# Optimization experiments

Measured on AMD Instinct MI355X. Metric: run time of the kernel, lower is better.

Reference implementation:

```python
import jax, jax.numpy as jnp
import numpy as np

THRESHOLD = 0.5
NEG_POS = 3
ALPHA = 1.0


def cxcy_to_xy(c):
    return jnp.concatenate([c[..., :2] - c[..., 2:] / 2, c[..., :2] + c[..., 2:] / 2], axis=-1)


def xy_to_cxcy(x):
    return jnp.concatenate([(x[..., :2] + x[..., 2:]) / 2, x[..., 2:] - x[..., :2]], axis=-1)


def encode_gcxgcy(cxcy, priors_cxcy):
    # SSD offset encoding with variances (10, 10, 5, 5)
    return jnp.concatenate([
        (cxcy[..., :2] - priors_cxcy[..., :2]) / (priors_cxcy[..., 2:] / 10.0),
        jnp.log(cxcy[..., 2:] / priors_cxcy[..., 2:]) * 5.0,
    ], axis=-1)


def compute_iou(a, b):
    # a: [n,4] xyxy, b: [m,4] xyxy -> [n,m]
    lt = jnp.maximum(a[:, None, :2], b[None, :, :2])
    rb = jnp.minimum(a[:, None, 2:], b[None, :, 2:])
    wh = jnp.clip(rb - lt, 0.0)
    inter = wh[..., 0] * wh[..., 1]
    area_a = (a[:, 2] - a[:, 0]) * (a[:, 3] - a[:, 1])
    area_b = (b[:, 2] - b[:, 0]) * (b[:, 3] - b[:, 1])
    return inter / (area_a[:, None] + area_b[None, :] - inter)


def _match_one(boxes, labels, db_xy, db_cxcy):
    # boxes: [n_obj,4] xyxy, labels: [n_obj], priors: [P,4]
    n_obj = boxes.shape[0]
    overlaps = compute_iou(boxes, db_xy)                 # [n_obj, P]
    ov_per_box = jnp.max(overlaps, axis=0)               # [P]
    obj_per_box = jnp.argmax(overlaps, axis=0)           # [P]
    box_per_obj = jnp.argmax(overlaps, axis=1)           # [n_obj]
    # force each gt to own its best prior
    obj_per_box = obj_per_box.at[box_per_obj].set(jnp.arange(n_obj))
    ov_per_box = ov_per_box.at[box_per_obj].set(1.0)
    lbl = labels[obj_per_box]                            # [P]
    lbl = jnp.where(ov_per_box < THRESHOLD, 0, lbl)      # background below threshold
    true_locs = encode_gcxgcy(xy_to_cxcy(boxes[obj_per_box]), db_cxcy)  # [P,4]
    return true_locs, lbl


def smooth_l1(x):
    ax = jnp.abs(x)
    return jnp.where(ax < 1.0, 0.5 * x * x, ax - 0.5)


def reference(loc_pred, cls_pred, gt_boxes, gt_labels, default_boxes):
    # loc_pred: [B,P,4], cls_pred: [B,P,C], gt_boxes: [B,n_obj,4],
    # gt_labels: [B,n_obj] int, default_boxes: [P,4] cxcywh
    db_xy = cxcy_to_xy(default_boxes)
    true_locs, true_labels = jax.vmap(_match_one, in_axes=(0, 0, None, None))(
        gt_boxes, gt_labels, db_xy, default_boxes)      # [B,P,4], [B,P]

    positive = true_labels > 0                           # [B,P]
    n_pos = jnp.sum(positive, axis=1)                    # [B]
    n_pos_total = jnp.sum(n_pos).astype(loc_pred.dtype)

    # localization loss: SmoothL1 mean over positive box elements
    loc_elem = smooth_l1(loc_pred - true_locs)           # [B,P,4]
    loc_loss = jnp.sum(loc_elem * positive[..., None]) / (n_pos_total * 4.0)

    # confidence loss: cross entropy with 3:1 hard negative mining
    logp = jax.nn.log_softmax(cls_pred, axis=-1)         # [B,P,C]
    ce = -jnp.take_along_axis(logp, true_labels[..., None], axis=-1)[..., 0]  # [B,P]
    conf_pos = jnp.sum(ce * positive)
    ce_neg = jnp.where(positive, 0.0, ce)
    # rank negatives by loss (descending) per image; take top neg_pos * n_pos
    ranks = jnp.argsort(jnp.argsort(-ce_neg, axis=1), axis=1)  # [B,P]
    hard_neg = ranks < (NEG_POS * n_pos)[:, None]
    conf_hard = jnp.sum(ce_neg * hard_neg)
    conf_loss = (conf_pos + conf_hard) / n_pos_total

    return conf_loss + ALPHA * loc_loss


def setup_inputs() -> dict:
    key = jax.random.key(0)
    ks = jax.random.split(key, 8)
    B, P, C, n_obj = 64, 8732, 81, 32

    # priors in cxcywh, valid in [0,1]
    db_cxy = jax.random.uniform(ks[0], (P, 2), minval=0.05, maxval=0.95)
    db_wh = jax.random.uniform(ks[1], (P, 2), minval=0.05, maxval=0.3)
    default_boxes = jnp.concatenate([db_cxy, db_wh], axis=-1).astype(jnp.float32)

    # gt boxes: valid xyxy built from centers and sizes
    g_cxy = jax.random.uniform(ks[2], (B, n_obj, 2), minval=0.2, maxval=0.8)
    g_wh = jax.random.uniform(ks[3], (B, n_obj, 2), minval=0.1, maxval=0.4)
    gt_boxes = jnp.concatenate([g_cxy - g_wh / 2, g_cxy + g_wh / 2], axis=-1).astype(jnp.float32)
    gt_labels = jax.random.randint(ks[4], (B, n_obj), 1, C)

    loc_pred = jax.random.normal(ks[5], (B, P, 4), dtype=jnp.float32) * 0.1
    cls_pred = jax.random.normal(ks[6], (B, P, C), dtype=jnp.float32)

    return {"loc_pred": loc_pred, "cls_pred": cls_pred, "gt_boxes": gt_boxes,
            "gt_labels": gt_labels, "default_boxes": default_boxes}
```

## Files before the change

### kernel.cpp

```cpp
#include <hip/hip_runtime.h>
#include <hip/hip_bf16.h>
#include <math.h>

#define BB 64
#define PP 8732
#define CC 81
#define NOBJ 32
#define CHUNKS ((PP + 255) / 256)
#define NPRI (BB * PP)
#define WTILE 16
#define WTW (WTILE * CC)
#define NWT (NPRI / WTILE)
#define CE_BLOCKS 1792

typedef float f4 __attribute__((ext_vector_type(4)));

__device__ __forceinline__ float sl1(float x) {
    float ax = fabsf(x);
    return (ax < 1.0f) ? 0.5f * x * x : ax - 0.5f;
}

__global__ __launch_bounds__(256) void k_bestprior(
    const float* __restrict__ gt_boxes,
    const float* __restrict__ dbox,
    int*   __restrict__ bp,
    float* __restrict__ acc,
    int*   __restrict__ npt,
    int*   __restrict__ done,
    int*   __restrict__ n_pos)
{
    __shared__ float s_bv[4];
    __shared__ int   s_bi[4];
    const int tid = threadIdx.x, lane = tid & 63, wave = tid >> 6;
    const int b = blockIdx.x >> 5;
    const int o = blockIdx.x & 31;

    if (blockIdx.x == 0) {
        if (tid < BB) n_pos[tid] = 0;
        else if (tid < BB + 3) acc[tid - BB] = 0.0f;
        else if (tid == BB + 3) *npt = 0;
        else if (tid == BB + 4) *done = 0;
    }

    const float* g = gt_boxes + (b * NOBJ + o) * 4;
    float gx0 = g[0], gy0 = g[1], gx1 = g[2], gy1 = g[3];
    float garea = (gx1 - gx0) * (gy1 - gy0);

    float best = -1.0f; int bpp = 0x7fffffff;
    for (int p = tid; p < PP; p += 256) {
        float4 db = reinterpret_cast<const float4*>(dbox)[p];
        float px0 = db.x - db.z * 0.5f, py0 = db.y - db.w * 0.5f;
        float px1 = db.x + db.z * 0.5f, py1 = db.y + db.w * 0.5f;
        float parea = db.z * db.w;
        float lx = fmaxf(px0, gx0), ly = fmaxf(py0, gy0);
        float rx = fminf(px1, gx1), ry = fminf(py1, gy1);
        float w = fmaxf(rx - lx, 0.0f), h = fmaxf(ry - ly, 0.0f);
        float inter = w * h;
        float iou = inter / (garea + parea - inter);
        if (iou > best) { best = iou; bpp = p; }
    }
#pragma unroll
    for (int m = 32; m > 0; m >>= 1) {
        float ov = __shfl_xor(best, m);
        int   op = __shfl_xor(bpp, m);
        if (ov > best || (ov == best && op < bpp)) { best = ov; bpp = op; }
    }
    if (lane == 0) { s_bv[wave] = best; s_bi[wave] = bpp; }
    __syncthreads();
    if (tid == 0) {
        for (int w2 = 1; w2 < 4; ++w2) {
            if (s_bv[w2] > best || (s_bv[w2] == best && s_bi[w2] < bpp)) {
                best = s_bv[w2]; bpp = s_bi[w2];
            }
        }
        bp[b * NOBJ + o] = bpp;
    }
}

__global__ __launch_bounds__(256) void k_assign(
    const float* __restrict__ loc_pred,
    const float* __restrict__ gt_boxes,
    const int*   __restrict__ gt_labels,
    const float* __restrict__ dbox,
    const int*   __restrict__ bp,
    int*   __restrict__ true_label,
    int*   __restrict__ n_pos,
    float* __restrict__ acc,
    int*   __restrict__ n_pos_total)
{
    __shared__ float s_gx0[NOBJ], s_gy0[NOBJ], s_gx1[NOBJ], s_gy1[NOBJ], s_garea[NOBJ];
    __shared__ float s_gcx[NOBJ], s_gcy[NOBJ], s_gw[NOBJ], s_gh[NOBJ];
    __shared__ int   s_glbl[NOBJ], s_bp[NOBJ];
    __shared__ float red_f[256];
    __shared__ int   red_i[256];

    const int b     = blockIdx.x / CHUNKS;
    const int chunk = blockIdx.x % CHUNKS;
    const int tid   = threadIdx.x;
    const int p     = chunk * 256 + tid;

    if (tid < NOBJ) {
        float x0 = gt_boxes[(b * NOBJ + tid) * 4 + 0];
        float y0 = gt_boxes[(b * NOBJ + tid) * 4 + 1];
        float x1 = gt_boxes[(b * NOBJ + tid) * 4 + 2];
        float y1 = gt_boxes[(b * NOBJ + tid) * 4 + 3];
        s_gx0[tid] = x0; s_gy0[tid] = y0; s_gx1[tid] = x1; s_gy1[tid] = y1;
        s_garea[tid] = (x1 - x0) * (y1 - y0);
        s_gcx[tid] = (x0 + x1) * 0.5f;
        s_gcy[tid] = (y0 + y1) * 0.5f;
        s_gw[tid]  = x1 - x0;
        s_gh[tid]  = y1 - y0;
        s_glbl[tid] = gt_labels[b * NOBJ + tid];
        s_bp[tid]   = bp[b * NOBJ + tid];
    }
    __syncthreads();

    float loc_local = 0.0f;
    int   np_local  = 0;

    if (p < PP) {
        float4 db = reinterpret_cast<const float4*>(dbox)[p];
        float px0 = db.x - db.z * 0.5f, py0 = db.y - db.w * 0.5f;
        float px1 = db.x + db.z * 0.5f, py1 = db.y + db.w * 0.5f;
        float parea = db.z * db.w;

        float best = -1.0f; int bo = 0;
#pragma unroll
        for (int o = 0; o < NOBJ; ++o) {
            float lx = fmaxf(px0, s_gx0[o]), ly = fmaxf(py0, s_gy0[o]);
            float rx = fminf(px1, s_gx1[o]), ry = fminf(py1, s_gy1[o]);
            float w = fmaxf(rx - lx, 0.0f), h = fmaxf(ry - ly, 0.0f);
            float inter = w * h;
            float iou = inter / (s_garea[o] + parea - inter);
            if (iou > best) { best = iou; bo = o; }
        }
        int forced = -1;
#pragma unroll
        for (int o = 0; o < NOBJ; ++o)
            if (s_bp[o] == p) forced = o;

        int o_use, lbl;
        if (forced >= 0) { o_use = forced; lbl = s_glbl[forced]; }
        else             { o_use = bo; lbl = (best < 0.5f) ? 0 : s_glbl[bo]; }

        true_label[b * PP + p] = lbl;
        if (lbl > 0) {
            np_local = 1;
            float g0 = (s_gcx[o_use] - db.x) / (db.z / 10.0f);
            float g1 = (s_gcy[o_use] - db.y) / (db.w / 10.0f);
            float g2 = logf(s_gw[o_use] / db.z) * 5.0f;
            float g3 = logf(s_gh[o_use] / db.w) * 5.0f;
            float4 lp = reinterpret_cast<const float4*>(loc_pred)[b * PP + p];
            loc_local = sl1(lp.x - g0) + sl1(lp.y - g1) + sl1(lp.z - g2) + sl1(lp.w - g3);
        }
    }

    red_f[tid] = loc_local;
    red_i[tid] = np_local;
    __syncthreads();
#pragma unroll
    for (int st = 128; st > 0; st >>= 1) {
        if (tid < st) { red_f[tid] += red_f[tid + st]; red_i[tid] += red_i[tid + st]; }
        __syncthreads();
    }
    if (tid == 0) {
        if (red_f[0] != 0.0f) atomicAdd(&acc[0], red_f[0]);
        if (red_i[0]) {
            atomicAdd(&n_pos[b], red_i[0]);
            atomicAdd(n_pos_total, red_i[0]);
        }
    }
}

__global__ __launch_bounds__(256) void k_ce(
    const float* __restrict__ cls_pred,
    const int*   __restrict__ true_label,
    float* __restrict__ ce_neg,
    float* __restrict__ acc)
{
    __shared__ float s_x[4][WTW];
    __shared__ float s_red[4];
    const int tid  = threadIdx.x;
    const int wave = tid >> 6, lane = tid & 63;
    const int rloc = lane >> 2, q = lane & 3;
    const int NW   = CE_BLOCKS * 4;

    float* sx = s_x[wave];
    f4* dst = reinterpret_cast<f4*>(sx);

    const float L2E = 1.4426950408889634f;
    const float LN2 = 0.6931471805599453f;
    float local = 0.0f;

    int wt = blockIdx.x * 4 + wave;
    f4 r0, r1, r2, r3, r4, r5;
    int lbl_next = 0;
    if (wt < NWT) {
        const f4* src = reinterpret_cast<const f4*>(cls_pred + (size_t)wt * WTW);
        r0 = __builtin_nontemporal_load(src + lane);
        r1 = __builtin_nontemporal_load(src + 64 + lane);
        r2 = __builtin_nontemporal_load(src + 128 + lane);
        r3 = __builtin_nontemporal_load(src + 192 + lane);
        r4 = __builtin_nontemporal_load(src + 256 + lane);
        if (lane < 4) r5 = __builtin_nontemporal_load(src + 320 + lane);
        lbl_next = true_label[wt * WTILE + rloc];
    }

    while (wt < NWT) {
        dst[lane] = r0; dst[64 + lane] = r1; dst[128 + lane] = r2;
        dst[192 + lane] = r3; dst[256 + lane] = r4;
        if (lane < 4) dst[320 + lane] = r5;
        const int lbl  = lbl_next;
        const int pidx = wt * WTILE + rloc;

        wt += NW;
        if (wt < NWT) {
            const f4* src = reinterpret_cast<const f4*>(cls_pred + (size_t)wt * WTW);
            r0 = __builtin_nontemporal_load(src + lane);
            r1 = __builtin_nontemporal_load(src + 64 + lane);
            r2 = __builtin_nontemporal_load(src + 128 + lane);
            r3 = __builtin_nontemporal_load(src + 192 + lane);
            r4 = __builtin_nontemporal_load(src + 256 + lane);
            if (lane < 4) r5 = __builtin_nontemporal_load(src + 320 + lane);
            lbl_next = true_label[wt * WTILE + rloc];
        }

        const float* x = sx + rloc * CC;
        const int base = q * 20;
        float s0 = 0.0f, s1 = 0.0f;
#pragma unroll
        for (int j = 0; j < 20; j += 2) {
            s0 += exp2f(x[base + j]     * L2E);
            s1 += exp2f(x[base + j + 1] * L2E);
        }
        float s = s0 + s1;
        if (q == 3) s += exp2f(x[80] * L2E);
        s += __shfl_xor(s, 1);
        s += __shfl_xor(s, 2);

        if (q == 0) {
            float ce = fmaf(log2f(s), LN2, -x[lbl]);
            ce_neg[pidx] = (lbl > 0) ? 0.0f : ce;
            local += (lbl > 0) ? ce : 0.0f;
        }
    }

#pragma unroll
    for (int m = 32; m > 0; m >>= 1) local += __shfl_xor(local, m);
    if (lane == 0) s_red[wave] = local;
    __syncthreads();
    if (tid == 0) {
        float tot = s_red[0] + s_red[1] + s_red[2] + s_red[3];
        if (tot != 0.0f) atomicAdd(&acc[1], tot);
    }
}

__global__ __launch_bounds__(1024) void k_select(
    const float* __restrict__ ce_neg,
    const int*   __restrict__ n_pos,
    float* __restrict__ acc,
    const int*  __restrict__ n_pos_total,
    int*   __restrict__ done,
    float* __restrict__ out)
{
    __shared__ unsigned int sv[PP];
    __shared__ unsigned int h16[16][256];
    __shared__ unsigned int hist[257];
    __shared__ unsigned int wtot[4];
    __shared__ unsigned int s_prefix, s_krem;
    __shared__ float rf[16];
    __shared__ int   ri[16];

    const int b = blockIdx.x, tid = threadIdx.x;
    const int lane = tid & 63, w = tid >> 6;

    int K = n_pos[b] * 3;
    if (K > PP) K = PP;

    if (K > 0) {
        for (int i = tid; i < PP; i += 1024)
            sv[i] = __float_as_uint(ce_neg[b * PP + i]);

        unsigned int prefix = 0, krem = (unsigned int)K;
        for (int shift = 24; shift >= 0; shift -= 8) {
            unsigned int* hflat = &h16[0][0];
            for (int j = tid; j < 16 * 256; j += 1024) hflat[j] = 0;
            if (tid == 0) hist[256] = 0;
            __syncthreads();
            unsigned int mask_hi = (shift == 24) ? 0u : (0xFFFFFFFFu << (shift + 8));
            for (int i = tid; i < PP; i += 1024) {
                unsigned int v = sv[i];
                if ((v & mask_hi) == prefix)
                    atomicAdd(&h16[w][(v >> shift) & 0xFFu], 1u);
            }
            __syncthreads();
            unsigned int s = 0;
            if (tid < 256) {
#pragma unroll
                for (int r = 0; r < 16; ++r) s += h16[r][tid];
#pragma unroll
                for (int off = 1; off < 64; off <<= 1) {
                    unsigned int a = __shfl_down(s, off);
                    if (lane + off < 64) s += a;
                }
                if (lane == 0) wtot[w] = s;
            }
            __syncthreads();
            if (tid < 256) {
                unsigned int sb = 0;
#pragma unroll
                for (int r = 0; r < 16; ++r) sb += h16[r][tid];
                unsigned int suf = sb;
#pragma unroll
                for (int off = 1; off < 64; off <<= 1) {
                    unsigned int a = __shfl_down(suf, off);
                    if (lane + off < 64) suf += a;
                }
                for (int w2 = w + 1; w2 < 4; ++w2) suf += wtot[w2];
                hist[tid] = suf;
            }
            __syncthreads();
            if (tid < 256) {
                unsigned int suf  = hist[tid];
                unsigned int suf1 = hist[tid + 1];
                if (suf >= krem && suf1 < krem) {
                    s_prefix = prefix | ((unsigned int)tid << shift);
                    s_krem   = krem - suf1;
                }
            }
            __syncthreads();
            prefix = s_prefix; krem = s_krem;
        }
        float cutoff = __uint_as_float(prefix);

        float sum_gt = 0.0f; int cnt_gt = 0;
        for (int i = tid; i < PP; i += 1024) {
            float v = __uint_as_float(sv[i]);
            if (v > cutoff) { sum_gt += v; cnt_gt++; }
        }
#pragma unroll
        for (int m = 32; m > 0; m >>= 1) {
            sum_gt += __shfl_xor(sum_gt, m);
            cnt_gt += __shfl_xor(cnt_gt, m);
        }
        if (lane == 0) { rf[w] = sum_gt; ri[w] = cnt_gt; }
        __syncthreads();
        if (tid == 0) {
            float sg = 0.0f; int cg = 0;
#pragma unroll
            for (int r = 0; r < 16; ++r) { sg += rf[r]; cg += ri[r]; }
            atomicAdd(&acc[2], sg + (float)(K - cg) * cutoff);
        }
    }

    if (tid == 0) {
        __threadfence();
        int old = atomicAdd(done, 1);
        if (old == BB - 1) {
            float a0 = atomicAdd(&acc[0], 0.0f);
            float a1 = atomicAdd(&acc[1], 0.0f);
            float a2 = atomicAdd(&acc[2], 0.0f);
            float npt = (float)atomicAdd((int*)n_pos_total, 0);
            out[0] = (a1 + a2) / npt + a0 / (npt * 4.0f);
        }
    }
}

extern "C" void kernel_launch(void* const* d_in, const int* in_sizes, int n_in,
                              void* d_out, int out_size, void* d_ws, size_t ws_size,
                              hipStream_t stream) {
    const float* loc_pred  = (const float*)d_in[0];
    const float* cls_pred  = (const float*)d_in[1];
    const float* gt_boxes  = (const float*)d_in[2];
    const int*   gt_labels = (const int*)d_in[3];
    const float* dbox      = (const float*)d_in[4];
    float* out = (float*)d_out;

    float* acc        = (float*)d_ws;
    int*   npt        = (int*)d_ws + 3;
    int*   done       = (int*)d_ws + 4;
    int*   n_pos      = (int*)d_ws + 8;
    int*   bp         = (int*)d_ws + 8 + BB;
    int*   true_label = (int*)d_ws + 8 + BB + BB * NOBJ;
    float* ce_neg     = (float*)(true_label + (size_t)NPRI);

    k_bestprior<<<BB * NOBJ, 256, 0, stream>>>(gt_boxes, dbox, bp,
                                               acc, npt, done, n_pos);
    k_assign<<<BB * CHUNKS, 256, 0, stream>>>(loc_pred, gt_boxes, gt_labels, dbox, bp,
                                              true_label, n_pos, acc, npt);
    k_ce<<<CE_BLOCKS, 256, 0, stream>>>(cls_pred, true_label, ce_neg, acc);
    k_select<<<BB, 1024, 0, stream>>>(ce_neg, n_pos, acc, npt, done, out);
}
```

Baseline: 150.6 us.

## Rewrite cross-entropy kernel so each lane reads four full rows directly

The CE kernel no longer stages 16-row tiles through LDS with a grid-stride prefetch loop. Each lane now loads four consecutive prior rows (81 floats each, 81 f4 loads) straight into registers and computes the log-sum-exp and label gather on its own, with one wave per 256 priors. This removes the LDS round trip, the quad shuffles and the loop overhead, and writes ce_neg as f4 stores. In exchange each lane's loads are strided by 1296 bytes, so coalescing is poorer, register pressure is higher, and many more blocks are launched, each doing a per-wave atomic.

Result: slower. 175.3 us (+16.4%).

```diff
diff --git a/kernel.cpp b/kernel.cpp
--- a/kernel.cpp
+++ b/kernel.cpp
@@ -8,10 +8,8 @@
 #define NOBJ 32
 #define CHUNKS ((PP + 255) / 256)
 #define NPRI (BB * PP)
-#define WTILE 16
-#define WTW (WTILE * CC)
-#define NWT (NPRI / WTILE)
-#define CE_BLOCKS 1792
+#define NWAVES (NPRI / 256)
+#define CE_BLOCKS ((NWAVES + 3) / 4)
 
 typedef float f4 __attribute__((ext_vector_type(4)));
 
@@ -178,81 +176,69 @@
     float* __restrict__ ce_neg,
     float* __restrict__ acc)
 {
-    __shared__ float s_x[4][WTW];
-    __shared__ float s_red[4];
-    const int tid  = threadIdx.x;
-    const int wave = tid >> 6, lane = tid & 63;
-    const int rloc = lane >> 2, q = lane & 3;
-    const int NW   = CE_BLOCKS * 4;
-
-    float* sx = s_x[wave];
-    f4* dst = reinterpret_cast<f4*>(sx);
+    const int tid = threadIdx.x, wave = tid >> 6, lane = tid & 63;
+    const int gw = blockIdx.x * 4 + wave;
+    if (gw >= NWAVES) return;
+
+    const int rb = gw * 256 + lane * 4;
+    const f4* src = reinterpret_cast<const f4*>(cls_pred + (size_t)rb * CC);
+    const int4 lb = *reinterpret_cast<const int4*>(true_label + rb);
+    const int l0 = lb.x, l1 = lb.y, l2 = lb.z, l3 = lb.w;
 
     const float L2E = 1.4426950408889634f;
     const float LN2 = 0.6931471805599453f;
-    float local = 0.0f;
-
-    int wt = blockIdx.x * 4 + wave;
-    f4 r0, r1, r2, r3, r4, r5;
-    int lbl_next = 0;
-    if (wt < NWT) {
-        const f4* src = reinterpret_cast<const f4*>(cls_pred + (size_t)wt * WTW);
-        r0 = __builtin_nontemporal_load(src + lane);
-        r1 = __builtin_nontemporal_load(src + 64 + lane);
-        r2 = __builtin_nontemporal_load(src + 128 + lane);
-        r3 = __builtin_nontemporal_load(src + 192 + lane);
-        r4 = __builtin_nontemporal_load(src + 256 + lane);
-        if (lane < 4) r5 = __builtin_nontemporal_load(src + 320 + lane);
-        lbl_next = true_label[wt * WTILE + rloc];
-    }
-
-    while (wt < NWT) {
-        dst[lane] = r0; dst[64 + lane] = r1; dst[128 + lane] = r2;
-        dst[192 + lane] = r3; dst[256 + lane] = r4;
-        if (lane < 4) dst[320 + lane] = r5;
-        const int lbl  = lbl_next;
-        const int pidx = wt * WTILE + rloc;
-
-        wt += NW;
-        if (wt < NWT) {
-            const f4* src = reinterpret_cast<const f4*>(cls_pred + (size_t)wt * WTW);
-            r0 = __builtin_nontemporal_load(src + lane);
-            r1 = __builtin_nontemporal_load(src + 64 + lane);
-            r2 = __builtin_nontemporal_load(src + 128 + lane);
-            r3 = __builtin_nontemporal_load(src + 192 + lane);
-            r4 = __builtin_nontemporal_load(src + 256 + lane);
-            if (lane < 4) r5 = __builtin_nontemporal_load(src + 320 + lane);
-            lbl_next = true_label[wt * WTILE + rloc];
-        }
-
-        const float* x = sx + rloc * CC;
-        const int base = q * 20;
-        float s0 = 0.0f, s1 = 0.0f;
-#pragma unroll
-        for (int j = 0; j < 20; j += 2) {
-            s0 += exp2f(x[base + j]     * L2E);
-            s1 += exp2f(x[base + j + 1] * L2E);
-        }
-        float s = s0 + s1;
-        if (q == 3) s += exp2f(x[80] * L2E);
-        s += __shfl_xor(s, 1);
-        s += __shfl_xor(s, 2);
-
-        if (q == 0) {
-            float ce = fmaf(log2f(s), LN2, -x[lbl]);
-            ce_neg[pidx] = (lbl > 0) ? 0.0f : ce;
-            local += (lbl > 0) ? ce : 0.0f;
-        }
-    }
-
-#pragma unroll
-    for (int m = 32; m > 0; m >>= 1) local += __shfl_xor(local, m);
-    if (lane == 0) s_red[wave] = local;
-    __syncthreads();
-    if (tid == 0) {
-        float tot = s_red[0] + s_red[1] + s_red[2] + s_red[3];
-        if (tot != 0.0f) atomicAdd(&acc[1], tot);
-    }
+
+    float s0 = 0.0f, s1 = 0.0f, s2 = 0.0f, s3 = 0.0f;
+    float xl0 = 0.0f, xl1 = 0.0f, xl2 = 0.0f, xl3 = 0.0f;
+    f4 v[16];
+
+#pragma unroll
+    for (int bb = 0; bb < 5; ++bb) {
+#pragma unroll
+        for (int j = 0; j < 16; ++j) v[j] = src[bb * 16 + j];
+#pragma unroll
+        for (int j = 0; j < 16; ++j) {
+#pragma unroll
+            for (int k = 0; k < 4; ++k) {
+                const int f = (bb * 16 + j) * 4 + k;
+                const int r = f / CC, c = f - r * CC;
+                float x = v[j][k];
+                float e = exp2f(x * L2E);
+                if      (r == 0) { s0 += e; if (c == l0) xl0 = x; }
+                else if (r == 1) { s1 += e; if (c == l1) xl1 = x; }
+                else if (r == 2) { s2 += e; if (c == l2) xl2 = x; }
+                else             { s3 += e; if (c == l3) xl3 = x; }
+            }
+        }
+    }
+    {
+        f4 vt = src[80];
+#pragma unroll
+        for (int k = 0; k < 4; ++k) {
+            const int c = 77 + k;
+            float x = vt[k];
+            s3 += exp2f(x * L2E);
+            if (c == l3) xl3 = x;
+        }
+    }
+
+    float ce0 = fmaf(log2f(s0), LN2, -xl0);
+    float ce1 = fmaf(log2f(s1), LN2, -xl1);
+    float ce2 = fmaf(log2f(s2), LN2, -xl2);
+    float ce3 = fmaf(log2f(s3), LN2, -xl3);
+
+    f4 outv;
+    outv.x = (l0 > 0) ? 0.0f : ce0;
+    outv.y = (l1 > 0) ? 0.0f : ce1;
+    outv.z = (l2 > 0) ? 0.0f : ce2;
+    outv.w = (l3 > 0) ? 0.0f : ce3;
+    reinterpret_cast<f4*>(ce_neg)[gw * 64 + lane] = outv;
+
+    float conf = ((l0 > 0) ? ce0 : 0.0f) + ((l1 > 0) ? ce1 : 0.0f)
+               + ((l2 > 0) ? ce2 : 0.0f) + ((l3 > 0) ? ce3 : 0.0f);
+#pragma unroll
+    for (int m = 32; m > 0; m >>= 1) conf += __shfl_xor(conf, m);
+    if (lane == 0 && conf != 0.0f) atomicAdd(&acc[1], conf);
 }
 
 __global__ __launch_bounds__(1024) void k_select(
```

## Compute label-independent logsumexp alongside best-prior search, fold CE into assign

Applied to the files above, without the earlier changes.

The cross-entropy pass over cls_pred no longer depends on the matched labels. It now runs inside the same launch as the best-prior search and stores logsumexp and x[0] per prior. The assign kernel then finishes CE using a gathered cls_pred[label] for positives and the stored x[0] for negatives. This removes one kernel launch and the serial dependency between assignment and the large class-score read, letting the bandwidth-bound LSE overlap the IoU search. In exchange it writes and reads an extra float2 per prior, does scattered gathers for positives, and clamps CE at zero with fmaxf.

Measured after the change: 160.8 us. 1.07x slower.

```diff
diff --git a/kernel.cpp b/kernel.cpp
--- a/kernel.cpp
+++ b/kernel.cpp
@@ -11,7 +11,9 @@
 #define WTILE 16
 #define WTW (WTILE * CC)
 #define NWT (NPRI / WTILE)
-#define CE_BLOCKS 1792
+#define LSE_BLOCKS 1792
+#define BP_BLOCKS (BB * NOBJ)
+#define PRE_BLOCKS (BP_BLOCKS + LSE_BLOCKS)
 
 typedef float f4 __attribute__((ext_vector_type(4)));
 
@@ -20,20 +22,22 @@
     return (ax < 1.0f) ? 0.5f * x * x : ax - 0.5f;
 }
 
-__global__ __launch_bounds__(256) void k_bestprior(
+__global__ __launch_bounds__(256) void k_pre(
     const float* __restrict__ gt_boxes,
     const float* __restrict__ dbox,
+    const float* __restrict__ cls_pred,
     int*   __restrict__ bp,
+    float* __restrict__ lsex0,
     float* __restrict__ acc,
     int*   __restrict__ npt,
     int*   __restrict__ done,
     int*   __restrict__ n_pos)
 {
+    __shared__ float s_x[4][WTW];
     __shared__ float s_bv[4];
     __shared__ int   s_bi[4];
-    const int tid = threadIdx.x, lane = tid & 63, wave = tid >> 6;
-    const int b = blockIdx.x >> 5;
-    const int o = blockIdx.x & 31;
+    const int tid  = threadIdx.x;
+    const int wave = tid >> 6, lane = tid & 63;
 
     if (blockIdx.x == 0) {
         if (tid < BB) n_pos[tid] = 0;
@@ -42,38 +46,102 @@
         else if (tid == BB + 4) *done = 0;
     }
 
-    const float* g = gt_boxes + (b * NOBJ + o) * 4;
-    float gx0 = g[0], gy0 = g[1], gx1 = g[2], gy1 = g[3];
-    float garea = (gx1 - gx0) * (gy1 - gy0);
-
-    float best = -1.0f; int bpp = 0x7fffffff;
-    for (int p = tid; p < PP; p += 256) {
-        float4 db = reinterpret_cast<const float4*>(dbox)[p];
-        float px0 = db.x - db.z * 0.5f, py0 = db.y - db.w * 0.5f;
-        float px1 = db.x + db.z * 0.5f, py1 = db.y + db.w * 0.5f;
-        float parea = db.z * db.w;
-        float lx = fmaxf(px0, gx0), ly = fmaxf(py0, gy0);
-        float rx = fminf(px1, gx1), ry = fminf(py1, gy1);
-        float w = fmaxf(rx - lx, 0.0f), h = fmaxf(ry - ly, 0.0f);
-        float inter = w * h;
-        float iou = inter / (garea + parea - inter);
-        if (iou > best) { best = iou; bpp = p; }
-    }
-#pragma unroll
-    for (int m = 32; m > 0; m >>= 1) {
-        float ov = __shfl_xor(best, m);
-        int   op = __shfl_xor(bpp, m);
-        if (ov > best || (ov == best && op < bpp)) { best = ov; bpp = op; }
-    }
-    if (lane == 0) { s_bv[wave] = best; s_bi[wave] = bpp; }
-    __syncthreads();
-    if (tid == 0) {
-        for (int w2 = 1; w2 < 4; ++w2) {
-            if (s_bv[w2] > best || (s_bv[w2] == best && s_bi[w2] < bpp)) {
-                best = s_bv[w2]; bpp = s_bi[w2];
-            }
-        }
-        bp[b * NOBJ + o] = bpp;
+    if (blockIdx.x < BP_BLOCKS) {
+        const int b = blockIdx.x >> 5;
+        const int o = blockIdx.x & 31;
+
+        const float* g = gt_boxes + (b * NOBJ + o) * 4;
+        float gx0 = g[0], gy0 = g[1], gx1 = g[2], gy1 = g[3];
+        float garea = (gx1 - gx0) * (gy1 - gy0);
+
+        float best = -1.0f; int bpp = 0x7fffffff;
+        for (int p = tid; p < PP; p += 256) {
+            float4 db = reinterpret_cast<const float4*>(dbox)[p];
+            float px0 = db.x - db.z * 0.5f, py0 = db.y - db.w * 0.5f;
+            float px1 = db.x + db.z * 0.5f, py1 = db.y + db.w * 0.5f;
+            float parea = db.z * db.w;
+            float lx = fmaxf(px0, gx0), ly = fmaxf(py0, gy0);
+            float rx = fminf(px1, gx1), ry = fminf(py1, gy1);
+            float w = fmaxf(rx - lx, 0.0f), h = fmaxf(ry - ly, 0.0f);
+            float inter = w * h;
+            float iou = inter / (garea + parea - inter);
+            if (iou > best) { best = iou; bpp = p; }
+        }
+#pragma unroll
+        for (int m = 32; m > 0; m >>= 1) {
+            float ov = __shfl_xor(best, m);
+            int   op = __shfl_xor(bpp, m);
+            if (ov > best || (ov == best && op < bpp)) { best = ov; bpp = op; }
+        }
+        if (lane == 0) { s_bv[wave] = best; s_bi[wave] = bpp; }
+        __syncthreads();
+        if (tid == 0) {
+            for (int w2 = 1; w2 < 4; ++w2) {
+                if (s_bv[w2] > best || (s_bv[w2] == best && s_bi[w2] < bpp)) {
+                    best = s_bv[w2]; bpp = s_bi[w2];
+                }
+            }
+            bp[b * NOBJ + o] = bpp;
+        }
+        return;
+    }
+
+    const int rloc = lane >> 2, q = lane & 3;
+    const int NW   = LSE_BLOCKS * 4;
+    float* sx = s_x[wave];
+    f4* dst = reinterpret_cast<f4*>(sx);
+
+    const float L2E = 1.4426950408889634f;
+    const float LN2 = 0.6931471805599453f;
+
+    int wt = (blockIdx.x - BP_BLOCKS) * 4 + wave;
+    f4 r0, r1, r2, r3, r4, r5;
+    if (wt < NWT) {
+        const f4* src = reinterpret_cast<const f4*>(cls_pred + (size_t)wt * WTW);
+        r0 = __builtin_nontemporal_load(src + lane);
+        r1 = __builtin_nontemporal_load(src + 64 + lane);
+        r2 = __builtin_nontemporal_load(src + 128 + lane);
+        r3 = __builtin_nontemporal_load(src + 192 + lane);
+        r4 = __builtin_nontemporal_load(src + 256 + lane);
+        if (lane < 4) r5 = __builtin_nontemporal_load(src + 320 + lane);
+    }
+
+    while (wt < NWT) {
+        dst[lane] = r0; dst[64 + lane] = r1; dst[128 + lane] = r2;
+        dst[192 + lane] = r3; dst[256 + lane] = r4;
+        if (lane < 4) dst[320 + lane] = r5;
+        const int pidx = wt * WTILE + rloc;
+
+        wt += NW;
+        if (wt < NWT) {
+            const f4* src = reinterpret_cast<const f4*>(cls_pred + (size_t)wt * WTW);
+            r0 = __builtin_nontemporal_load(src + lane);
+            r1 = __builtin_nontemporal_load(src + 64 + lane);
+            r2 = __builtin_nontemporal_load(src + 128 + lane);
+            r3 = __builtin_nontemporal_load(src + 192 + lane);
+            r4 = __builtin_nontemporal_load(src + 256 + lane);
+            if (lane < 4) r5 = __builtin_nontemporal_load(src + 320 + lane);
+        }
+
+        const float* x = sx + rloc * CC;
+        const int base = q * 20;
+        float s0 = 0.0f, s1 = 0.0f;
+#pragma unroll
+        for (int j = 0; j < 20; j += 2) {
+            s0 += exp2f(x[base + j]     * L2E);
+            s1 += exp2f(x[base + j + 1] * L2E);
+        }
+        float s = s0 + s1;
+        if (q == 3) s += exp2f(x[80] * L2E);
+        s += __shfl_xor(s, 1);
+        s += __shfl_xor(s, 2);
+
+        if (q == 0) {
+            float2 o;
+            o.x = log2f(s) * LN2;
+            o.y = x[0];
+            reinterpret_cast<float2*>(lsex0)[pidx] = o;
+        }
     }
 }
 
@@ -83,7 +151,9 @@
     const int*   __restrict__ gt_labels,
     const float* __restrict__ dbox,
     const int*   __restrict__ bp,
-    int*   __restrict__ true_label,
+    const float* __restrict__ cls_pred,
+    const float* __restrict__ lsex0,
+    float* __restrict__ ce_neg,
     int*   __restrict__ n_pos,
     float* __restrict__ acc,
     int*   __restrict__ n_pos_total)
@@ -91,7 +161,7 @@
     __shared__ float s_gx0[NOBJ], s_gy0[NOBJ], s_gx1[NOBJ], s_gy1[NOBJ], s_garea[NOBJ];
     __shared__ float s_gcx[NOBJ], s_gcy[NOBJ], s_gw[NOBJ], s_gh[NOBJ];
     __shared__ int   s_glbl[NOBJ], s_bp[NOBJ];
-    __shared__ float red_f[256];
+    __shared__ float red_f[256], red_g[256];
     __shared__ int   red_i[256];
 
     const int b     = blockIdx.x / CHUNKS;
@@ -115,10 +185,11 @@
     }
     __syncthreads();
 
-    float loc_local = 0.0f;
+    float loc_local = 0.0f, pos_local = 0.0f;
     int   np_local  = 0;
 
     if (p < PP) {
+        const int idx = b * PP + p;
         float4 db = reinterpret_cast<const float4*>(dbox)[p];
         float px0 = db.x - db.z * 0.5f, py0 = db.y - db.w * 0.5f;
         float px1 = db.x + db.z * 0.5f, py1 = db.y + db.w * 0.5f;
@@ -143,115 +214,44 @@
         if (forced >= 0) { o_use = forced; lbl = s_glbl[forced]; }
         else             { o_use = bo; lbl = (best < 0.5f) ? 0 : s_glbl[bo]; }
 
-        true_label[b * PP + p] = lbl;
+        float2 lx0 = reinterpret_cast<const float2*>(lsex0)[idx];
+
         if (lbl > 0) {
             np_local = 1;
+            ce_neg[idx] = 0.0f;
+            float xl = cls_pred[(size_t)idx * CC + lbl];
+            pos_local = fmaxf(lx0.x - xl, 0.0f);
             float g0 = (s_gcx[o_use] - db.x) / (db.z / 10.0f);
             float g1 = (s_gcy[o_use] - db.y) / (db.w / 10.0f);
             float g2 = logf(s_gw[o_use] / db.z) * 5.0f;
             float g3 = logf(s_gh[o_use] / db.w) * 5.0f;
-            float4 lp = reinterpret_cast<const float4*>(loc_pred)[b * PP + p];
+            float4 lp = reinterpret_cast<const float4*>(loc_pred)[idx];
             loc_local = sl1(lp.x - g0) + sl1(lp.y - g1) + sl1(lp.z - g2) + sl1(lp.w - g3);
+        } else {
+            ce_neg[idx] = fmaxf(lx0.x - lx0.y, 0.0f);
         }
     }
 
     red_f[tid] = loc_local;
+    red_g[tid] = pos_local;
     red_i[tid] = np_local;
     __syncthreads();
 #pragma unroll
     for (int st = 128; st > 0; st >>= 1) {
-        if (tid < st) { red_f[tid] += red_f[tid + st]; red_i[tid] += red_i[tid + st]; }
+        if (tid < st) {
+            red_f[tid] += red_f[tid + st];
+            red_g[tid] += red_g[tid + st];
+            red_i[tid] += red_i[tid + st];
+        }
         __syncthreads();
     }
     if (tid == 0) {
         if (red_f[0] != 0.0f) atomicAdd(&acc[0], red_f[0]);
+        if (red_g[0] != 0.0f) atomicAdd(&acc[1], red_g[0]);
         if (red_i[0]) {
             atomicAdd(&n_pos[b], red_i[0]);
             atomicAdd(n_pos_total, red_i[0]);
         }
-    }
-}
-
-__global__ __launch_bounds__(256) void k_ce(
-    const float* __restrict__ cls_pred,
-    const int*   __restrict__ true_label,
-    float* __restrict__ ce_neg,
-    float* __restrict__ acc)
-{
-    __shared__ float s_x[4][WTW];
-    __shared__ float s_red[4];
-    const int tid  = threadIdx.x;
-    const int wave = tid >> 6, lane = tid & 63;
-    const int rloc = lane >> 2, q = lane & 3;
-    const int NW   = CE_BLOCKS * 4;
-
-    float* sx = s_x[wave];
-    f4* dst = reinterpret_cast<f4*>(sx);
-
-    const float L2E = 1.4426950408889634f;
-    const float LN2 = 0.6931471805599453f;
-    float local = 0.0f;
-
-    int wt = blockIdx.x * 4 + wave;
-    f4 r0, r1, r2, r3, r4, r5;
-    int lbl_next = 0;
-    if (wt < NWT) {
-        const f4* src = reinterpret_cast<const f4*>(cls_pred + (size_t)wt * WTW);
-        r0 = __builtin_nontemporal_load(src + lane);
-        r1 = __builtin_nontemporal_load(src + 64 + lane);
-        r2 = __builtin_nontemporal_load(src + 128 + lane);
-        r3 = __builtin_nontemporal_load(src + 192 + lane);
-        r4 = __builtin_nontemporal_load(src + 256 + lane);
-        if (lane < 4) r5 = __builtin_nontemporal_load(src + 320 + lane);
-        lbl_next = true_label[wt * WTILE + rloc];
-    }
-
-    while (wt < NWT) {
-        dst[lane] = r0; dst[64 + lane] = r1; dst[128 + lane] = r2;
-        dst[192 + lane] = r3; dst[256 + lane] = r4;
-        if (lane < 4) dst[320 + lane] = r5;
-        const int lbl  = lbl_next;
-        const int pidx = wt * WTILE + rloc;
-
-        wt += NW;
-        if (wt < NWT) {
-            const f4* src = reinterpret_cast<const f4*>(cls_pred + (size_t)wt * WTW);
-            r0 = __builtin_nontemporal_load(src + lane);
-            r1 = __builtin_nontemporal_load(src + 64 + lane);
-            r2 = __builtin_nontemporal_load(src + 128 + lane);
-            r3 = __builtin_nontemporal_load(src + 192 + lane);
-            r4 = __builtin_nontemporal_load(src + 256 + lane);
-            if (lane < 4) r5 = __builtin_nontemporal_load(src + 320 + lane);
-            lbl_next = true_label[wt * WTILE + rloc];
-        }
-
-        const float* x = sx + rloc * CC;
-        const int base = q * 20;
-        float s0 = 0.0f, s1 = 0.0f;
-#pragma unroll
-        for (int j = 0; j < 20; j += 2) {
-            s0 += exp2f(x[base + j]     * L2E);
-            s1 += exp2f(x[base + j + 1] * L2E);
-        }
-        float s = s0 + s1;
-        if (q == 3) s += exp2f(x[80] * L2E);
-        s += __shfl_xor(s, 1);
-        s += __shfl_xor(s, 2);
-
-        if (q == 0) {
-            float ce = fmaf(log2f(s), LN2, -x[lbl]);
-            ce_neg[pidx] = (lbl > 0) ? 0.0f : ce;
-            local += (lbl > 0) ? ce : 0.0f;
-        }
-    }
-
-#pragma unroll
-    for (int m = 32; m > 0; m >>= 1) local += __shfl_xor(local, m);
-    if (lane == 0) s_red[wave] = local;
-    __syncthreads();
-    if (tid == 0) {
-        float tot = s_red[0] + s_red[1] + s_red[2] + s_red[3];
-        if (tot != 0.0f) atomicAdd(&acc[1], tot);
     }
 }
 
@@ -376,18 +376,17 @@
     const float* dbox      = (const float*)d_in[4];
     float* out = (float*)d_out;
 
-    float* acc        = (float*)d_ws;
-    int*   npt        = (int*)d_ws + 3;
-    int*   done       = (int*)d_ws + 4;
-    int*   n_pos      = (int*)d_ws + 8;
-    int*   bp         = (int*)d_ws + 8 + BB;
-    int*   true_label = (int*)d_ws + 8 + BB + BB * NOBJ;
-    float* ce_neg     = (float*)(true_label + (size_t)NPRI);
-
-    k_bestprior<<<BB * NOBJ, 256, 0, stream>>>(gt_boxes, dbox, bp,
-                                               acc, npt, done, n_pos);
+    float* acc    = (float*)d_ws;
+    int*   npt    = (int*)d_ws + 3;
+    int*   done   = (int*)d_ws + 4;
+    int*   n_pos  = (int*)d_ws + 8;
+    int*   bp     = (int*)d_ws + 8 + BB;
+    float* lsex0  = (float*)((int*)d_ws + 8 + BB + BB * NOBJ);
+    float* ce_neg = lsex0 + (size_t)2 * NPRI;
+
+    k_pre<<<PRE_BLOCKS, 256, 0, stream>>>(gt_boxes, dbox, cls_pred,
+                                          bp, lsex0, acc, npt, done, n_pos);
     k_assign<<<BB * CHUNKS, 256, 0, stream>>>(loc_pred, gt_boxes, gt_labels, dbox, bp,
-                                              true_label, n_pos, acc, npt);
-    k_ce<<<CE_BLOCKS, 256, 0, stream>>>(cls_pred, true_label, ce_neg, acc);
+                                              cls_pred, lsex0, ce_neg, n_pos, acc, npt);
     k_select<<<BB, 1024, 0, stream>>>(ce_neg, n_pos, acc, npt, done, out);
 }
```

## Double-buffer CE tile loads and vectorize LDS reads in softmax-CE kernel

Applied to the files above, without the earlier changes.

The cross-entropy kernel now keeps two tiles of class logits in flight per wave, with A/B register sets prefetching two iterations ahead to hide global memory latency. Shared-memory reads for the exp-sum are turned into six aligned float4 loads per lane, with edge lanes masked, instead of scalar reads. The block count and launch bounds are retuned to fit the extra registers. This raises register pressure and could lower occupancy.

Measured after the change: 169.4 us. +12.5%, slower.

```diff
diff --git a/kernel.cpp b/kernel.cpp
--- a/kernel.cpp
+++ b/kernel.cpp
@@ -11,7 +11,7 @@
 #define WTILE 16
 #define WTW (WTILE * CC)
 #define NWT (NPRI / WTILE)
-#define CE_BLOCKS 1792
+#define CE_BLOCKS 1536
 
 typedef float f4 __attribute__((ext_vector_type(4)));
 
@@ -172,7 +172,46 @@
     }
 }
 
-__global__ __launch_bounds__(256) void k_ce(
+#define CE_BODY(R0, R1, R2, R3, R4, R5, LBL)                                     \
+    {                                                                            \
+        dst[lane] = R0; dst[64 + lane] = R1; dst[128 + lane] = R2;               \
+        dst[192 + lane] = R3; dst[256 + lane] = R4;                              \
+        if (lane < 4) dst[320 + lane] = R5;                                      \
+        const int lbl  = LBL;                                                    \
+        const int pidx = wt * WTILE + rloc;                                      \
+        const int wtn  = wt + 2 * NW;                                            \
+        if (wtn < NWT) {                                                         \
+            const f4* src = reinterpret_cast<const f4*>(cls_pred + (size_t)wtn * WTW); \
+            R0 = __builtin_nontemporal_load(src + lane);                         \
+            R1 = __builtin_nontemporal_load(src + 64 + lane);                    \
+            R2 = __builtin_nontemporal_load(src + 128 + lane);                   \
+            R3 = __builtin_nontemporal_load(src + 192 + lane);                   \
+            R4 = __builtin_nontemporal_load(src + 256 + lane);                   \
+            if (lane < 4) R5 = __builtin_nontemporal_load(src + 320 + lane);     \
+            LBL = true_label[wtn * WTILE + rloc];                                \
+        }                                                                        \
+        f4 w0 = tile4[ws],     w1 = tile4[ws + 1], w2 = tile4[ws + 2];           \
+        f4 w3 = tile4[ws + 3], w4 = tile4[ws + 4], w5 = tile4[ws + 5];           \
+        float s0 = 0.0f, s1 = 0.0f;                                              \
+        _Pragma("unroll") for (int k = 0; k < 4; ++k) {                          \
+            float e = exp2f(w0[k] * L2E); s0 += (k >= a) ? e : 0.0f; }           \
+        _Pragma("unroll") for (int k = 0; k < 4; ++k) s1 += exp2f(w1[k] * L2E);  \
+        _Pragma("unroll") for (int k = 0; k < 4; ++k) s0 += exp2f(w2[k] * L2E);  \
+        _Pragma("unroll") for (int k = 0; k < 4; ++k) s1 += exp2f(w3[k] * L2E);  \
+        _Pragma("unroll") for (int k = 0; k < 4; ++k) s0 += exp2f(w4[k] * L2E);  \
+        _Pragma("unroll") for (int k = 0; k < 4; ++k) {                          \
+            float e = exp2f(w5[k] * L2E); s1 += (k < hi_cnt) ? e : 0.0f; }       \
+        float s = s0 + s1;                                                       \
+        s += __shfl_xor(s, 1);                                                   \
+        s += __shfl_xor(s, 2);                                                   \
+        if (q == 0) {                                                            \
+            float ce = fmaf(log2f(s), LN2, -sx[rloc * CC + lbl]);                \
+            ce_neg[pidx] = (lbl > 0) ? 0.0f : ce;                                \
+            local += (lbl > 0) ? ce : 0.0f;                                      \
+        }                                                                        \
+    }
+
+__global__ __launch_bounds__(256, 6) void k_ce(
     const float* __restrict__ cls_pred,
     const int*   __restrict__ true_label,
     float* __restrict__ ce_neg,
@@ -187,62 +226,50 @@
 
     float* sx = s_x[wave];
     f4* dst = reinterpret_cast<f4*>(sx);
+    const f4* tile4 = reinterpret_cast<const f4*>(sx);
+
+    const int seg_start = rloc * CC + q * 20;
+    const int seg_len   = (q == 3) ? 21 : 20;
+    const int ws        = seg_start >> 2;
+    const int a         = seg_start & 3;
+    const int hi_cnt    = a + seg_len - 20;
 
     const float L2E = 1.4426950408889634f;
     const float LN2 = 0.6931471805599453f;
     float local = 0.0f;
 
-    int wt = blockIdx.x * 4 + wave;
-    f4 r0, r1, r2, r3, r4, r5;
-    int lbl_next = 0;
-    if (wt < NWT) {
-        const f4* src = reinterpret_cast<const f4*>(cls_pred + (size_t)wt * WTW);
-        r0 = __builtin_nontemporal_load(src + lane);
-        r1 = __builtin_nontemporal_load(src + 64 + lane);
-        r2 = __builtin_nontemporal_load(src + 128 + lane);
-        r3 = __builtin_nontemporal_load(src + 192 + lane);
-        r4 = __builtin_nontemporal_load(src + 256 + lane);
-        if (lane < 4) r5 = __builtin_nontemporal_load(src + 320 + lane);
-        lbl_next = true_label[wt * WTILE + rloc];
-    }
-
+    const int wt0 = blockIdx.x * 4 + wave;
+    f4 rA0, rA1, rA2, rA3, rA4, rA5;
+    f4 rB0, rB1, rB2, rB3, rB4, rB5;
+    int lblA, lblB;
+
+    {
+        const f4* srcA = reinterpret_cast<const f4*>(cls_pred + (size_t)wt0 * WTW);
+        rA0 = __builtin_nontemporal_load(srcA + lane);
+        rA1 = __builtin_nontemporal_load(srcA + 64 + lane);
+        rA2 = __builtin_nontemporal_load(srcA + 128 + lane);
+        rA3 = __builtin_nontemporal_load(srcA + 192 + lane);
+        rA4 = __builtin_nontemporal_load(srcA + 256 + lane);
+        if (lane < 4) rA5 = __builtin_nontemporal_load(srcA + 320 + lane);
+        lblA = true_label[wt0 * WTILE + rloc];
+
+        const f4* srcB = reinterpret_cast<const f4*>(cls_pred + (size_t)(wt0 + NW) * WTW);
+        rB0 = __builtin_nontemporal_load(srcB + lane);
+        rB1 = __builtin_nontemporal_load(srcB + 64 + lane);
+        rB2 = __builtin_nontemporal_load(srcB + 128 + lane);
+        rB3 = __builtin_nontemporal_load(srcB + 192 + lane);
+        rB4 = __builtin_nontemporal_load(srcB + 256 + lane);
+        if (lane < 4) rB5 = __builtin_nontemporal_load(srcB + 320 + lane);
+        lblB = true_label[(wt0 + NW) * WTILE + rloc];
+    }
+
+    int wt = wt0;
     while (wt < NWT) {
-        dst[lane] = r0; dst[64 + lane] = r1; dst[128 + lane] = r2;
-        dst[192 + lane] = r3; dst[256 + lane] = r4;
-        if (lane < 4) dst[320 + lane] = r5;
-        const int lbl  = lbl_next;
-        const int pidx = wt * WTILE + rloc;
-
+        CE_BODY(rA0, rA1, rA2, rA3, rA4, rA5, lblA)
         wt += NW;
-        if (wt < NWT) {
-            const f4* src = reinterpret_cast<const f4*>(cls_pred + (size_t)wt * WTW);
-            r0 = __builtin_nontemporal_load(src + lane);
-            r1 = __builtin_nontemporal_load(src + 64 + lane);
-            r2 = __builtin_nontemporal_load(src + 128 + lane);
-            r3 = __builtin_nontemporal_load(src + 192 + lane);
-            r4 = __builtin_nontemporal_load(src + 256 + lane);
-            if (lane < 4) r5 = __builtin_nontemporal_load(src + 320 + lane);
-            lbl_next = true_label[wt * WTILE + rloc];
-        }
-
-        const float* x = sx + rloc * CC;
-        const int base = q * 20;
-        float s0 = 0.0f, s1 = 0.0f;
-#pragma unroll
-        for (int j = 0; j < 20; j += 2) {
-            s0 += exp2f(x[base + j]     * L2E);
-            s1 += exp2f(x[base + j + 1] * L2E);
-        }
-        float s = s0 + s1;
-        if (q == 3) s += exp2f(x[80] * L2E);
-        s += __shfl_xor(s, 1);
-        s += __shfl_xor(s, 2);
-
-        if (q == 0) {
-            float ce = fmaf(log2f(s), LN2, -x[lbl]);
-            ce_neg[pidx] = (lbl > 0) ? 0.0f : ce;
-            local += (lbl > 0) ? ce : 0.0f;
-        }
+        if (wt >= NWT) break;
+        CE_BODY(rB0, rB1, rB2, rB3, rB4, rB5, lblB)
+        wt += NW;
     }
 
 #pragma unroll
@@ -300,8 +327,8 @@
                 for (int r = 0; r < 16; ++r) s += h16[r][tid];
 #pragma unroll
                 for (int off = 1; off < 64; off <<= 1) {
-                    unsigned int a = __shfl_down(s, off);
-                    if (lane + off < 64) s += a;
+                    unsigned int aa = __shfl_down(s, off);
+                    if (lane + off < 64) s += aa;
                 }
                 if (lane == 0) wtot[w] = s;
             }
@@ -313,8 +340,8 @@
                 unsigned int suf = sb;
 #pragma unroll
                 for (int off = 1; off < 64; off <<= 1) {
-                    unsigned int a = __shfl_down(suf, off);
-                    if (lane + off < 64) suf += a;
+                    unsigned int aa = __shfl_down(suf, off);
+                    if (lane + off < 64) suf += aa;
                 }
                 for (int w2 = w + 1; w2 < 4; ++w2) suf += wtot[w2];
                 hist[tid] = suf;
```
